# Kernel optimization log

Measured on AMD Instinct MI355X. Metric: run time of the kernel, lower is better.

The kernel has to match this reference:

```python
import jax, jax.numpy as jnp
import numpy as np

DMODEL = 512
NUM_HEADS = 8
DK = DMODEL // NUM_HEADS  # 64
CAUSAL = True


def setup_inputs() -> dict:
    key = jax.random.key(0)
    ks = jax.random.split(key, 11)
    B, S = 4, 2048
    s_in = 1.0 / np.sqrt(DMODEL)
    s_out = 1.0 / np.sqrt(NUM_HEADS * DK)
    return {
        "Q": jax.random.normal(ks[0], (B, S, DMODEL), jnp.float32),
        "K": jax.random.normal(ks[1], (B, S, DMODEL), jnp.float32),
        "V": jax.random.normal(ks[2], (B, S, DMODEL), jnp.float32),
        # torch nn.Linear weights stored as [in, out] (already transposed)
        "WQ_w": jax.random.uniform(ks[3], (DMODEL, DK), jnp.float32, -s_in, s_in),
        "WQ_b": jax.random.uniform(ks[4], (DK,), jnp.float32, -s_in, s_in),
        "WK_w": jax.random.uniform(ks[5], (DMODEL, DK), jnp.float32, -s_in, s_in),
        "WK_b": jax.random.uniform(ks[6], (DK,), jnp.float32, -s_in, s_in),
        "WV_w": jax.random.uniform(ks[7], (DMODEL, DK), jnp.float32, -s_in, s_in),
        "WV_b": jax.random.uniform(ks[8], (DK,), jnp.float32, -s_in, s_in),
        "Wo_w": jax.random.uniform(ks[9], (NUM_HEADS * DK, DMODEL), jnp.float32, -s_out, s_out),
        "Wo_b": jax.random.uniform(ks[10], (DMODEL,), jnp.float32, -s_out, s_out),
    }


def reference(Q, K, V, WQ_w, WQ_b, WK_w, WK_b, WV_w, WV_b, Wo_w, Wo_b):
    # Single shared projection to dk=64 (NOT per-head in the original module)
    q = Q @ WQ_w + WQ_b  # [B,S,dk]
    k = K @ WK_w + WK_b  # [B,S,dk]
    v = V @ WV_w + WV_b  # [B,S,dk]
    scores = jnp.einsum("bsd,btd->bst", q, k) / np.sqrt(DK).astype(np.float32)
    if CAUSAL:
        S = scores.shape[-1]
        causal = jnp.tril(jnp.ones((S, S), dtype=bool))  # True = keep
        scores = jnp.where(causal, scores, -jnp.inf)
    attn = jax.nn.softmax(scores, axis=-1)
    head_out = jnp.einsum("bst,btd->bsd", attn, v)  # [B,S,dk]
    # Every head is identical -> concat == tile num_heads copies
    concat = jnp.tile(head_out, (1, 1, NUM_HEADS))  # [B,S,num_heads*dk]
    return concat @ Wo_w + Wo_b  # [B,S,dmodel]
```

## Files before the change

kernel.cpp:

```cpp
#include <hip/hip_runtime.h>

#define DMODEL 512
#define DK 64
#define NH 8
#define SEQ 2048
#define BATCH 4
#define NEGBIG -1.0e30f
#define SPLITW 8
#define DKP 66
#define SHIFT2 8.656170245f
#define QSCALE 0.1803368801f

typedef _Float16 half_t;
typedef _Float16 half4 __attribute__((ext_vector_type(4)));
typedef _Float16 half8 __attribute__((ext_vector_type(8)));
typedef float floatx4 __attribute__((ext_vector_type(4)));

#ifdef __has_builtin
#  if __has_builtin(__builtin_amdgcn_exp2f)
#    define EXP2F(x) __builtin_amdgcn_exp2f(x)
#  endif
#  if __has_builtin(__builtin_amdgcn_cvt_pkrtz)
#    define HAVE_PKRTZ 1
#  endif
#  if __has_builtin(__builtin_amdgcn_mfma_f32_16x16x16f16)
#    define HAVE_MFMA16 1
#  endif
#endif
#ifndef EXP2F
#  define EXP2F(x) exp2f(x)
#endif
#ifndef HAVE_PKRTZ
#  define HAVE_PKRTZ 0
#endif
#ifndef HAVE_MFMA16
#  define HAVE_MFMA16 0
#endif

__device__ __forceinline__ half4 pk4(const float* p) {
#if HAVE_PKRTZ
    half4 r;
    auto lo = __builtin_amdgcn_cvt_pkrtz(p[0], p[1]);
    auto hi = __builtin_amdgcn_cvt_pkrtz(p[2], p[3]);
    __builtin_memcpy(&r, &lo, 4);
    __builtin_memcpy(reinterpret_cast<char*>(&r) + 4, &hi, 4);
    return r;
#else
    return (half4){(half_t)p[0], (half_t)p[1], (half_t)p[2], (half_t)p[3]};
#endif
}

__global__ __launch_bounds__(128) void proj_kernel(
    const float* __restrict__ Q, const float* __restrict__ K, const float* __restrict__ V,
    const float* __restrict__ WQ, const float* __restrict__ WK, const float* __restrict__ WV,
    const float* __restrict__ Wo,
    const float* __restrict__ bQ, const float* __restrict__ bK, const float* __restrict__ bV,
    half_t* __restrict__ qh, half_t* __restrict__ kh, half_t* __restrict__ vt,
    half_t* __restrict__ wo_tr)
{
    const int tens = blockIdx.y;
    const int tid = threadIdx.x;

    if (tens == 3) {
        const int bx = blockIdx.x;
        if (bx >= 256) return;
        const int idx = bx * 128 + tid;
        const int n2 = idx & 511;
        const int k2 = idx >> 9;
        float s = 0.f;
#pragma unroll
        for (int h = 0; h < NH; h++)
            s += Wo[((size_t)(h * DK + k2)) * DMODEL + n2];
        wo_tr[(size_t)n2 * DK + k2] = (half_t)s;
        return;
    }

    const float* __restrict__ X  = (tens == 0) ? Q : (tens == 1) ? K : V;
    const float* __restrict__ Wf = (tens == 0) ? WQ : (tens == 1) ? WK : WV;
    const float* __restrict__ bias = (tens == 0) ? bQ : (tens == 1) ? bK : bV;

    const int r0 = blockIdx.x * 16;
    const int w = tid >> 6;
    const int lane = tid & 63;
    const int c = lane & 15;
    const int quad = lane >> 4;

    __shared__ floatx4 red[4][64];

    floatx4 acc[4] = {{0.f,0.f,0.f,0.f},{0.f,0.f,0.f,0.f},{0.f,0.f,0.f,0.f},{0.f,0.f,0.f,0.f}};

    const float* xrow = X + (size_t)(r0 + c) * DMODEL + quad * 8;
#pragma unroll 8
    for (int ks = w; ks < 16; ks += 2) {
        const float* xp = xrow + ks * 32;
        half8 a;
#pragma unroll
        for (int i = 0; i < 8; i++) a[i] = (half_t)xp[i];
        const float* wbase = Wf + (size_t)(ks * 32 + quad * 8) * DK + c;
#pragma unroll
        for (int nt = 0; nt < 4; nt++) {
            half8 bfr;
#pragma unroll
            for (int j = 0; j < 8; j++)
                bfr[j] = (half_t)wbase[(size_t)j * DK + nt * 16];
            acc[nt] = __builtin_amdgcn_mfma_f32_16x16x32_f16(a, bfr, acc[nt], 0, 0, 0);
        }
    }

    if (w == 1) {
#pragma unroll
        for (int nt = 0; nt < 4; nt++) red[nt][lane] = acc[nt];
    }
    __syncthreads();
    if (w == 1) return;

#pragma unroll
    for (int nt = 0; nt < 4; nt++) {
        const floatx4 r4 = red[nt][lane];
        const float bv = bias[nt * 16 + c];
#pragma unroll
        for (int r = 0; r < 4; r++) {
            const float val = acc[nt][r] + r4[r] + bv;
            const int row = r0 + quad * 4 + r;
            if (tens == 0) {
                qh[(size_t)row * DK + nt * 16 + c] = (half_t)(val * QSCALE);
            } else if (tens == 1) {
                kh[(size_t)row * DK + nt * 16 + c] = (half_t)val;
            } else {
                const int b  = row >> 11;
                const int s  = row & (SEQ - 1);
                const int kb = s >> 4;
                const int kk = s & 15;
                vt[(size_t)(b * 128 + kb) * 1024
                   + (size_t)c * 64 + (nt >> 1) * 32 + (kk >> 2) * 8 + (nt & 1) * 4 + (kk & 3)]
                    = (half_t)val;
            }
        }
    }
}

__global__ __launch_bounds__(512, 4) void attn_kernel(
    const half_t* __restrict__ qh, const half_t* __restrict__ kh,
    const half_t* __restrict__ vt, const half_t* __restrict__ wo_tr,
    const float* __restrict__ bo, float* __restrict__ out)
{
    const int bx = blockIdx.x;
    int b, qt;
    if (bx < 256) { qt = bx >> 1;            b = bx & 1; }
    else          { int k2 = bx - 256; qt = 127 - (k2 >> 1); b = 2 + (k2 & 1); }
    const int tid = threadIdx.x;
    const int w = tid >> 6;
    const int lane = tid & 63;
    const int c = lane & 15;
    const int quad = lane >> 4;

    __shared__ float sow[SPLITW][16][DKP];
    __shared__ float sl_s[SPLITW][16];
    __shared__ half_t of16[16][72];

    const half_t* qrow = qh + (size_t)(b * SEQ + qt * 16 + c) * DK + quad * 8;
    half8 qb0 = *(const half8*)(qrow);
    half8 qb1 = *(const half8*)(qrow + 32);

    float lp = 0.f;
    floatx4 o[4] = {{0.f,0.f,0.f,0.f},{0.f,0.f,0.f,0.f},{0.f,0.f,0.f,0.f},{0.f,0.f,0.f,0.f}};
    const floatx4 cinit = {-SHIFT2, -SHIFT2, -SHIFT2, -SHIFT2};

    const half_t* kbb = kh + (size_t)b * SEQ * DK;
    const half_t* vtb = vt + (size_t)b * 128 * 1024;

    int pb = w;
    half8 ka0, ka1, kb0, kb1;
    if (2 * pb <= qt) {
        const half_t* kr0 = kbb + (size_t)(2 * pb * 16 + c) * DK + quad * 8;
        ka0 = *(const half8*)(kr0);
        ka1 = *(const half8*)(kr0 + 32);
        const half_t* kr1 = kr0 + 16 * DK;
        kb0 = *(const half8*)(kr1);
        kb1 = *(const half8*)(kr1 + 32);
    }

    while (2 * pb <= qt) {
        const int t0 = 2 * pb, t1 = 2 * pb + 1;
        const half_t* vp0 = vtb + (size_t)t0 * 1024 + c * 64 + quad * 8;
        const half_t* vp1 = vtb + (size_t)t1 * 1024 + c * 64 + quad * 8;
        half8 va01 = *(const half8*)(vp0);
        half8 va23 = *(const half8*)(vp0 + 32);
        half8 vc01 = *(const half8*)(vp1);
        half8 vc23 = *(const half8*)(vp1 + 32);

        const int npb = pb + SPLITW;
        half8 nka0 = ka0, nka1 = ka1, nkb0 = kb0, nkb1 = kb1;
        if (2 * npb <= qt) {
            const half_t* nkr0 = kbb + (size_t)(2 * npb * 16 + c) * DK + quad * 8;
            nka0 = *(const half8*)(nkr0);
            nka1 = *(const half8*)(nkr0 + 32);
            const half_t* nkr1 = nkr0 + 16 * DK;
            nkb0 = *(const half8*)(nkr1);
            nkb1 = *(const half8*)(nkr1 + 32);
        }

        floatx4 sc0 = cinit;
        sc0 = __builtin_amdgcn_mfma_f32_16x16x32_f16(ka0, qb0, sc0, 0, 0, 0);
        sc0 = __builtin_amdgcn_mfma_f32_16x16x32_f16(ka1, qb1, sc0, 0, 0, 0);
        floatx4 sc1 = cinit;
        sc1 = __builtin_amdgcn_mfma_f32_16x16x32_f16(kb0, qb0, sc1, 0, 0, 0);
        sc1 = __builtin_amdgcn_mfma_f32_16x16x32_f16(kb1, qb1, sc1, 0, 0, 0);

        if (t0 == qt) {
#pragma unroll
            for (int r = 0; r < 4; r++) {
                if (quad * 4 + r > c) sc0[r] = NEGBIG;
                sc1[r] = NEGBIG;
            }
        } else if (t1 == qt) {
#pragma unroll
            for (int r = 0; r < 4; r++)
                if (quad * 4 + r > c) sc1[r] = NEGBIG;
        }

        float p0[4], p1[4];
#pragma unroll
        for (int r = 0; r < 4; r++) { p0[r] = EXP2F(sc0[r]); p1[r] = EXP2F(sc1[r]); }
        lp += (p0[0] + p0[1]) + (p0[2] + p0[3]) + ((p1[0] + p1[1]) + (p1[2] + p1[3]));

#if HAVE_MFMA16
        half4 pa = pk4(p0), pc = pk4(p1);
        half4 va0 = __builtin_shufflevector(va01, va01, 0, 1, 2, 3);
        half4 va1 = __builtin_shufflevector(va01, va01, 4, 5, 6, 7);
        half4 va2 = __builtin_shufflevector(va23, va23, 0, 1, 2, 3);
        half4 va3 = __builtin_shufflevector(va23, va23, 4, 5, 6, 7);
        half4 vc0 = __builtin_shufflevector(vc01, vc01, 0, 1, 2, 3);
        half4 vc1 = __builtin_shufflevector(vc01, vc01, 4, 5, 6, 7);
        half4 vc2 = __builtin_shufflevector(vc23, vc23, 0, 1, 2, 3);
        half4 vc3 = __builtin_shufflevector(vc23, vc23, 4, 5, 6, 7);
        o[0] = __builtin_amdgcn_mfma_f32_16x16x16f16(pa, va0, o[0], 0, 0, 0);
        o[1] = __builtin_amdgcn_mfma_f32_16x16x16f16(pa, va1, o[1], 0, 0, 0);
        o[2] = __builtin_amdgcn_mfma_f32_16x16x16f16(pa, va2, o[2], 0, 0, 0);
        o[3] = __builtin_amdgcn_mfma_f32_16x16x16f16(pa, va3, o[3], 0, 0, 0);
        o[0] = __builtin_amdgcn_mfma_f32_16x16x16f16(pc, vc0, o[0], 0, 0, 0);
        o[1] = __builtin_amdgcn_mfma_f32_16x16x16f16(pc, vc1, o[1], 0, 0, 0);
        o[2] = __builtin_amdgcn_mfma_f32_16x16x16f16(pc, vc2, o[2], 0, 0, 0);
        o[3] = __builtin_amdgcn_mfma_f32_16x16x16f16(pc, vc3, o[3], 0, 0, 0);
#else
        half8 pa8, pc8;
#pragma unroll
        for (int jj = 0; jj < 8; jj++) {
            const int src = (((quad * 2 + (jj >> 2)) & 3) * 16 + c);
            const float pj0 = __shfl(p0[jj & 3], src);
            const float pj1 = __shfl(p1[jj & 3], src);
            pa8[jj] = (quad < 2) ? (half_t)pj0 : (half_t)0.f;
            pc8[jj] = (quad < 2) ? (half_t)pj1 : (half_t)0.f;
        }
#pragma unroll
        for (int nt = 0; nt < 4; nt++) {
            const half_t* vb0 = vtb + (size_t)t0 * 1024 + c * 64 + (nt >> 1) * 32 + (quad & 1) * 16 + (nt & 1) * 4;
            half4 l0 = *(const half4*)(vb0);
            half4 h0 = *(const half4*)(vb0 + 8);
            half8 v80 = {l0[0], l0[1], l0[2], l0[3], h0[0], h0[1], h0[2], h0[3]};
            o[nt] = __builtin_amdgcn_mfma_f32_16x16x32_f16(pa8, v80, o[nt], 0, 0, 0);
            const half_t* vb1 = vtb + (size_t)t1 * 1024 + c * 64 + (nt >> 1) * 32 + (quad & 1) * 16 + (nt & 1) * 4;
            half4 l1 = *(const half4*)(vb1);
            half4 h1 = *(const half4*)(vb1 + 8);
            half8 v81 = {l1[0], l1[1], l1[2], l1[3], h1[0], h1[1], h1[2], h1[3]};
            o[nt] = __builtin_amdgcn_mfma_f32_16x16x32_f16(pc8, v81, o[nt], 0, 0, 0);
        }
#endif
        ka0 = nka0; ka1 = nka1; kb0 = nkb0; kb1 = nkb1; pb = npb;
    }

    lp += __shfl_xor(lp, 16);
    lp += __shfl_xor(lp, 32);

#pragma unroll
    for (int nt = 0; nt < 4; nt++)
#pragma unroll
        for (int r = 0; r < 4; r++)
            sow[w][quad * 4 + r][nt * 16 + c] = o[nt][r];
    if (quad == 0) sl_s[w][c] = lp;
    __syncthreads();

    {
        const int q = w * 2 + (lane >> 5);
        const int d0 = (lane & 31) * 2;
        float lstar = 0.f, acc0 = 0.f, acc1 = 0.f;
#pragma unroll
        for (int ww = 0; ww < SPLITW; ww++) {
            lstar += sl_s[ww][q];
            const float* sp = &sow[ww][q][d0];
            acc0 += sp[0];
            acc1 += sp[1];
        }
        const float linv = 1.f / lstar;
        of16[q][d0]     = (half_t)(acc0 * linv);
        of16[q][d0 + 1] = (half_t)(acc1 * linv);
    }
    __syncthreads();

    half8 a1 = *(const half8*)(&of16[c][quad * 8]);
    half8 a2 = *(const half8*)(&of16[c][32 + quad * 8]);
    const size_t orow = (size_t)(b * SEQ + qt * 16);
#pragma unroll
    for (int i = 0; i < 4; i++) {
        const int n = (w * 4 + i) * 16 + c;
        half8 b1 = *(const half8*)(wo_tr + (size_t)n * DK + quad * 8);
        half8 b2 = *(const half8*)(wo_tr + (size_t)n * DK + 32 + quad * 8);
        floatx4 oc = {0.f, 0.f, 0.f, 0.f};
        oc = __builtin_amdgcn_mfma_f32_16x16x32_f16(a1, b1, oc, 0, 0, 0);
        oc = __builtin_amdgcn_mfma_f32_16x16x32_f16(a2, b2, oc, 0, 0, 0);
        const float bv = bo[n];
#pragma unroll
        for (int r = 0; r < 4; r++)
            out[(orow + quad * 4 + r) * DMODEL + n] = oc[r] + bv;
    }
}

extern "C" void kernel_launch(void* const* d_in, const int* in_sizes, int n_in,
                              void* d_out, int out_size, void* d_ws, size_t ws_size,
                              hipStream_t stream) {
    const float* Q  = (const float*)d_in[0];
    const float* K  = (const float*)d_in[1];
    const float* V  = (const float*)d_in[2];
    const float* WQ = (const float*)d_in[3];
    const float* bQ = (const float*)d_in[4];
    const float* WK = (const float*)d_in[5];
    const float* bK = (const float*)d_in[6];
    const float* WV = (const float*)d_in[7];
    const float* bV = (const float*)d_in[8];
    const float* Wo = (const float*)d_in[9];
    const float* bo = (const float*)d_in[10];
    float* out = (float*)d_out;

    char* ws = (char*)d_ws;
    half_t* qh    = (half_t*)ws;
    half_t* kh    = (half_t*)(ws + (1u << 20));
    half_t* vt    = (half_t*)(ws + (2u << 20));
    half_t* wo_tr = (half_t*)(ws + (3u << 20));

    proj_kernel<<<dim3(512, 4), 128, 0, stream>>>(
        Q, K, V, WQ, WK, WV, Wo, bQ, bK, bV, qh, kh, vt, wo_tr);
    attn_kernel<<<512, 512, 0, stream>>>(qh, kh, vt, wo_tr, bo, out);
}
```

Baseline: 141.5 us.

## Stage projection input rows in LDS with coalesced nontemporal loads, 32 rows per block

```diff
diff --git a/kernel.cpp b/kernel.cpp
--- a/kernel.cpp
+++ b/kernel.cpp
@@ -8,6 +8,7 @@
 #define NEGBIG -1.0e30f
 #define SPLITW 8
 #define DKP 66
+#define XSP 520
 #define SHIFT2 8.656170245f
 #define QSCALE 0.1803368801f
 
@@ -62,9 +63,7 @@
     const int tid = threadIdx.x;
 
     if (tens == 3) {
-        const int bx = blockIdx.x;
-        if (bx >= 256) return;
-        const int idx = bx * 128 + tid;
+        const int idx = blockIdx.x * 128 + tid;
         const int n2 = idx & 511;
         const int k2 = idx >> 9;
         float s = 0.f;
@@ -79,23 +78,41 @@
     const float* __restrict__ Wf = (tens == 0) ? WQ : (tens == 1) ? WK : WV;
     const float* __restrict__ bias = (tens == 0) ? bQ : (tens == 1) ? bK : bV;
 
-    const int r0 = blockIdx.x * 16;
+    const int r0 = blockIdx.x * 32;
     const int w = tid >> 6;
     const int lane = tid & 63;
     const int c = lane & 15;
     const int quad = lane >> 4;
 
-    __shared__ floatx4 red[4][64];
-
-    floatx4 acc[4] = {{0.f,0.f,0.f,0.f},{0.f,0.f,0.f,0.f},{0.f,0.f,0.f,0.f},{0.f,0.f,0.f,0.f}};
-
-    const float* xrow = X + (size_t)(r0 + c) * DMODEL + quad * 8;
+    __shared__ half_t xs[32][XSP];
+    __shared__ floatx4 red[2][4][64];
+
+    {
+        const floatx4* __restrict__ Xv = (const floatx4*)(X + (size_t)r0 * DMODEL);
+#pragma unroll
+        for (int batch = 0; batch < 4; batch++) {
+            floatx4 v[8];
+#pragma unroll
+            for (int j = 0; j < 8; j++)
+                v[j] = __builtin_nontemporal_load(&Xv[(batch * 8 + j) * 128 + tid]);
+#pragma unroll
+            for (int j = 0; j < 8; j++) {
+                const int fi = (batch * 8 + j) * 128 + tid;
+                half_t* d = &xs[fi >> 7][(fi & 127) * 4];
+                d[0] = (half_t)v[j][0]; d[1] = (half_t)v[j][1];
+                d[2] = (half_t)v[j][2]; d[3] = (half_t)v[j][3];
+            }
+        }
+    }
+    __syncthreads();
+
+    floatx4 acc[2][4] = {{{0.f,0.f,0.f,0.f},{0.f,0.f,0.f,0.f},{0.f,0.f,0.f,0.f},{0.f,0.f,0.f,0.f}},
+                         {{0.f,0.f,0.f,0.f},{0.f,0.f,0.f,0.f},{0.f,0.f,0.f,0.f},{0.f,0.f,0.f,0.f}}};
+
 #pragma unroll 8
     for (int ks = w; ks < 16; ks += 2) {
-        const float* xp = xrow + ks * 32;
-        half8 a;
-#pragma unroll
-        for (int i = 0; i < 8; i++) a[i] = (half_t)xp[i];
+        const half8 a0 = *(const half8*)(&xs[c][ks * 32 + quad * 8]);
+        const half8 a1 = *(const half8*)(&xs[16 + c][ks * 32 + quad * 8]);
         const float* wbase = Wf + (size_t)(ks * 32 + quad * 8) * DK + c;
 #pragma unroll
         for (int nt = 0; nt < 4; nt++) {
@@ -103,37 +120,43 @@
 #pragma unroll
             for (int j = 0; j < 8; j++)
                 bfr[j] = (half_t)wbase[(size_t)j * DK + nt * 16];
-            acc[nt] = __builtin_amdgcn_mfma_f32_16x16x32_f16(a, bfr, acc[nt], 0, 0, 0);
+            acc[0][nt] = __builtin_amdgcn_mfma_f32_16x16x32_f16(a0, bfr, acc[0][nt], 0, 0, 0);
+            acc[1][nt] = __builtin_amdgcn_mfma_f32_16x16x32_f16(a1, bfr, acc[1][nt], 0, 0, 0);
         }
     }
 
     if (w == 1) {
 #pragma unroll
-        for (int nt = 0; nt < 4; nt++) red[nt][lane] = acc[nt];
+        for (int rt = 0; rt < 2; rt++)
+#pragma unroll
+            for (int nt = 0; nt < 4; nt++) red[rt][nt][lane] = acc[rt][nt];
     }
     __syncthreads();
     if (w == 1) return;
 
 #pragma unroll
-    for (int nt = 0; nt < 4; nt++) {
-        const floatx4 r4 = red[nt][lane];
-        const float bv = bias[nt * 16 + c];
-#pragma unroll
-        for (int r = 0; r < 4; r++) {
-            const float val = acc[nt][r] + r4[r] + bv;
-            const int row = r0 + quad * 4 + r;
-            if (tens == 0) {
-                qh[(size_t)row * DK + nt * 16 + c] = (half_t)(val * QSCALE);
-            } else if (tens == 1) {
-                kh[(size_t)row * DK + nt * 16 + c] = (half_t)val;
-            } else {
-                const int b  = row >> 11;
-                const int s  = row & (SEQ - 1);
-                const int kb = s >> 4;
-                const int kk = s & 15;
-                vt[(size_t)(b * 128 + kb) * 1024
-                   + (size_t)c * 64 + (nt >> 1) * 32 + (kk >> 2) * 8 + (nt & 1) * 4 + (kk & 3)]
-                    = (half_t)val;
+    for (int rt = 0; rt < 2; rt++) {
+#pragma unroll
+        for (int nt = 0; nt < 4; nt++) {
+            const floatx4 r4 = red[rt][nt][lane];
+            const float bv = bias[nt * 16 + c];
+#pragma unroll
+            for (int r = 0; r < 4; r++) {
+                const float val = acc[rt][nt][r] + r4[r] + bv;
+                const int row = r0 + rt * 16 + quad * 4 + r;
+                if (tens == 0) {
+                    qh[(size_t)row * DK + nt * 16 + c] = (half_t)(val * QSCALE);
+                } else if (tens == 1) {
+                    kh[(size_t)row * DK + nt * 16 + c] = (half_t)val;
+                } else {
+                    const int b  = row >> 11;
+                    const int s  = row & (SEQ - 1);
+                    const int kb = s >> 4;
+                    const int kk = s & 15;
+                    vt[(size_t)(b * 128 + kb) * 1024
+                       + (size_t)c * 64 + (nt >> 1) * 32 + (kk >> 2) * 8 + (nt & 1) * 4 + (kk & 3)]
+                        = (half_t)val;
+                }
             }
         }
     }
@@ -311,7 +334,7 @@
         const float bv = bo[n];
 #pragma unroll
         for (int r = 0; r < 4; r++)
-            out[(orow + quad * 4 + r) * DMODEL + n] = oc[r] + bv;
+            __builtin_nontemporal_store(oc[r] + bv, &out[(orow + quad * 4 + r) * DMODEL + n]);
     }
 }
 
@@ -337,7 +360,7 @@
     half_t* vt    = (half_t*)(ws + (2u << 20));
     half_t* wo_tr = (half_t*)(ws + (3u << 20));
 
-    proj_kernel<<<dim3(512, 4), 128, 0, stream>>>(
+    proj_kernel<<<dim3(256, 4), 128, 0, stream>>>(
         Q, K, V, WQ, WK, WV, Wo, bQ, bK, bV, qh, kh, vt, wo_tr);
     attn_kernel<<<512, 512, 0, stream>>>(qh, kh, vt, wo_tr, bo, out);
 }
```

Result: faster. 136.4 us (-3.6%).
